# Kernel tuning notes

Hardware: AMD Instinct MI355X
Metric: run time of the kernel (lower is better)

## Reference

```python
import jax, jax.numpy as jnp
import numpy as np

B, C, G, Q, OUT = 2, 96, 32, 32, 45
M_FREQS = 12
SIGMA = 3.0


def _fourier_encode(c):
    # c: [..., 3]; log-linear frequency bank scaled by SIGMA (sigma**(j/m))
    m = M_FREQS
    freqs = SIGMA ** (jnp.arange(m, dtype=c.dtype) / m)          # [m]
    ang = 2.0 * jnp.pi * c[..., None] * freqs                    # [..., 3, m]
    enc = jnp.concatenate([jnp.sin(ang), jnp.cos(ang)], axis=-1)  # [..., 3, 2m]
    return enc.reshape(c.shape[:-1] + (3 * 2 * m,))


def setup_inputs():
    key = jax.random.key(0)
    ks = jax.random.split(key, 10)
    d = {}
    d["context_v"] = jax.random.normal(ks[0], (B, C, G, G, G), jnp.float32)
    g = jnp.arange(G, dtype=jnp.float32)
    grid = jnp.stack(jnp.meshgrid(g, g, g, indexing="ij"), axis=-1)  # [G,G,G,3]
    d["context_world_coord_grid"] = jnp.broadcast_to(grid, (B, G, G, G, 3))
    # queries strictly inside the grid so floor()+1 <= G-1
    d["query_world_coord"] = jax.random.uniform(ks[1], (B, Q, Q, Q, 3), jnp.float32, 0.0, G - 1.001)
    d["query_world_coord_mask"] = jnp.ones((B, Q, Q, Q, 1), dtype=bool)
    eye = jnp.broadcast_to(jnp.eye(4, dtype=jnp.float32), (B, 4, 4))
    d["affine_context_vox2world"] = eye
    d["affine_query_vox2world"] = eye
    d["context_vox_size_world"] = jnp.ones((B, 3), jnp.float32)
    d["query_vox_size_world"] = jnp.ones((B, 3), jnp.float32)

    n_coord = 6 + 3 * 2 * M_FREQS  # 78
    internal = C + n_coord         # 174

    def lin(k, fi, fo):
        s = 1.0 / np.sqrt(fi)
        kw, kb = jax.random.split(k)
        return (jax.random.uniform(kw, (fi, fo), jnp.float32, -s, s),
                jax.random.uniform(kb, (fo,), jnp.float32, -s, s))

    pk = jax.random.split(ks[2], 7)
    d["w00"], d["b00"] = lin(pk[0], internal, C)
    d["w01"], d["b01"] = lin(pk[1], C, C)
    d["w02"], d["b02"] = lin(pk[2], C, C)
    d["w10"], d["b10"] = lin(pk[3], internal, C)
    d["w11"], d["b11"] = lin(pk[4], C, C)
    d["w12"], d["b12"] = lin(pk[5], C, C)
    d["w_post"], d["b_post"] = lin(pk[6], C, OUT)
    return d


def reference(context_v, context_world_coord_grid, query_world_coord,
              query_world_coord_mask, affine_context_vox2world,
              affine_query_vox2world, context_vox_size_world,
              query_vox_size_world, w00, b00, w01, b01, w02, b02,
              w10, b10, w11, b11, w12, b12, w_post, b_post):
    Bq = context_v.shape[0]
    qshape = query_world_coord.shape
    qw = query_world_coord.reshape(Bq, -1, 3)          # [B,N,3]
    N = qw.shape[1]
    qm = query_world_coord_mask.reshape(Bq, -1, 1)     # [B,N,1]
    dummy = qw[:, N // 2][:, None]                      # [B,1,3]
    qw = jnp.where(qm, qw, dummy)

    inv = jnp.linalg.inv(affine_context_vox2world)
    q_vox = jnp.einsum("brc,bnc->bnr", inv[:, :3, :3], qw) + inv[:, None, :3, 3]
    bottom = jnp.floor(q_vox).astype(jnp.int32)         # [B,N,3]
    sub = q_vox - bottom.astype(q_vox.dtype)

    cvt = jnp.transpose(context_v, (0, 2, 3, 4, 1))     # [B,X,Y,Z,C]
    bidx = jnp.arange(Bq)[:, None]
    maskf = qm.astype(q_vox.dtype)
    blocks = ((w00, b00, w01, b01, w02, b02), (w10, b10, w11, b11, w12, b12))
    acc = jnp.zeros((Bq, N, w_post.shape[1]), q_vox.dtype)

    for oi in (0, 1):
        for oj in (0, 1):
            for ok in (0, 1):
                off_i = jnp.array([oi, oj, ok], dtype=bottom.dtype)
                idx = bottom + off_i                    # [B,N,3]
                feats = cvt[bidx, idx[..., 0], idx[..., 1], idx[..., 2]] * maskf  # [B,N,C]
                cw = context_world_coord_grid[bidx, idx[..., 0], idx[..., 1], idx[..., 2]]  # [B,N,3]
                off_f = off_i.astype(q_vox.dtype)
                rel = (sub - off_f + 1.0) / 2.0
                enc = _fourier_encode(rel)              # [B,N,72]
                coord = jnp.concatenate([cw, qw, enc], axis=-1) * maskf  # [B,N,78]
                y = feats
                for (wa, ba, wb, bb, wc, bc) in blocks:  # SkipMLPBlock x2
                    h = jnp.concatenate([y, coord], axis=-1)
                    h = jax.nn.silu(h @ wa + ba)
                    h = jax.nn.silu(h @ wb + bb)
                    h = jax.nn.silu(h @ wc + bc)
                    y = y + h
                pred = y @ w_post + b_post              # [B,N,OUT]
                compl = jnp.abs(1.0 - off_f)
                w_tri = jnp.prod(jnp.abs(bottom.astype(q_vox.dtype) + compl - q_vox), axis=-1, keepdims=True)
                acc = acc + w_tri * pred

    out = jnp.transpose(acc, (0, 2, 1)).reshape((Bq, w_post.shape[1]) + qshape[1:-1])
    return out
```

## Files before the change

### kernel.cpp

```cpp
#include <hip/hip_runtime.h>

#define NQv   32768
#define GSH   9216
#define NGRP  9
#define WTOT  (GSH*NGRP)
#define ASTR  104
#define CSTR  80
#define WBLK  325

typedef __attribute__((ext_vector_type(8))) short  short8;
typedef __attribute__((ext_vector_type(4))) float  float4v;

__device__ __forceinline__ float bfu2f(unsigned short u) {
  return __uint_as_float(((unsigned int)u) << 16);
}
__device__ __forceinline__ unsigned short f2bfu(float f) {
  unsigned int x = __float_as_uint(f);
  x += 0x7fffu + ((x >> 16) & 1u);
  return (unsigned short)(x >> 16);
}
__device__ __forceinline__ unsigned int rnd16(float f) {
  return __float_as_uint(f) + 0x8000u;
}
__device__ __forceinline__ unsigned int pkp(float lo, float hi) {
  return __builtin_amdgcn_perm(rnd16(hi), rnd16(lo), 0x07060302u);
}
__device__ __forceinline__ float silu_f(float x) {
  float e = __expf(-x);
  return x * __builtin_amdgcn_rcpf(1.f + e);
}
__device__ __forceinline__ int clamp31(int v) { return min(max(v, 0), 31); }

__device__ __forceinline__ void gload_lds16(const void* g, void* l) {
  typedef const __attribute__((address_space(1))) unsigned int GU;
  typedef __attribute__((address_space(3))) unsigned int LU;
  __builtin_amdgcn_global_load_lds((GU*)g, (LU*)l, 16, 0, 0);
}

__global__ __launch_bounds__(256) void prep_kernel(
    const float* __restrict__ ctxv,
    const float* __restrict__ w00, const float* __restrict__ w01,
    const float* __restrict__ w02, const float* __restrict__ w10,
    const float* __restrict__ w11, const float* __restrict__ w12,
    const float* __restrict__ wpost,
    const float* __restrict__ b00, const float* __restrict__ b10,
    unsigned short* __restrict__ ws, unsigned short* __restrict__ ctxvt)
{
  __shared__ float tile[96][65];
  const int blk0 = blockIdx.x;
  const int t = threadIdx.x;
  if (blk0 < WBLK) {
    int e = blk0 * 256 + t;
    if (e >= WTOT) {
      int e2 = e - WTOT;
      if (e2 < 192) {
        int mat = e2 / 96, ch = e2 - mat * 96;
        const float* w = mat ? w10 : w00;
        const float* bb = mat ? b10 : b00;
        float s = bb[ch];
#pragma unroll
        for (int k = 0; k < 6; ++k) s += 15.5f * w[(96 + k) * 96 + ch];
        ((float*)(ws + WTOT))[e2] = s;
      }
      return;
    }
    int g = e / GSH, r = e - g * GSH;
    int T = r >> 9, c = (r >> 3) & 63, e8 = r & 7;
    int mt = T / 3, cb = T - mt * 3;
    int ln15 = c >> 2, quad = c & 3;
    int n = mt * 16 + ln15;
    int kk = cb * 32 + quad * 8 + e8;
    const float* src; int Ksrc, Nsrc, kofs;
    switch (g) {
      case 0:  src = w00;   Ksrc = 174; Nsrc = 96; kofs = 0;  break;
      case 1:  src = w00;   Ksrc = 174; Nsrc = 96; kofs = 96; break;
      case 2:  src = w01;   Ksrc = 96;  Nsrc = 96; kofs = 0;  break;
      case 3:  src = w02;   Ksrc = 96;  Nsrc = 96; kofs = 0;  break;
      case 4:  src = w10;   Ksrc = 174; Nsrc = 96; kofs = 0;  break;
      case 5:  src = w10;   Ksrc = 174; Nsrc = 96; kofs = 96; break;
      case 6:  src = w11;   Ksrc = 96;  Nsrc = 96; kofs = 0;  break;
      case 7:  src = w12;   Ksrc = 96;  Nsrc = 96; kofs = 0;  break;
      default: src = wpost; Ksrc = 96;  Nsrc = 45; kofs = 0;  break;
    }
    int k = kofs + kk;
    float v = (k < Ksrc && n < Nsrc) ? src[k * Nsrc + n] : 0.f;
    ws[e] = f2bfu(v);
    return;
  }
  const int blk = blk0 - WBLK;
  const int b = blk >> 9, s0 = (blk & 511) << 6;
  const int cq = t >> 6, sl = t & 63;
#pragma unroll
  for (int p = 0; p < 24; ++p) {
    int c = cq + p * 4;
    tile[c][sl] = ctxv[(((size_t)(b * 96 + c)) << 15) + s0 + sl];
  }
  __syncthreads();
#pragma unroll
  for (int i = 0; i < 24; ++i) {
    int u = t + 256 * i;
    int s = u / 96, c = u - s * 96;
    ctxvt[((size_t)(b << 15) + s0 + s) * 96 + c] = f2bfu(tile[c][s]);
  }
}

template<int NM, bool INIT, bool BREG>
__device__ __forceinline__ void run_group(
    const short* __restrict__ sWp,
    const short* pA, const short8 (&Bin)[3][2],
    const float* __restrict__ bias, int biasN,
    float4v (&C)[NM][2], int lane, int rowb)
{
  const int ln15 = lane & 15, quad = lane >> 4;
  const int cidx = ((ln15 << 2) | quad) << 3;
  if (INIT) {
    if (biasN >= NM * 16) {
#pragma unroll
      for (int mt = 0; mt < NM; ++mt) {
        float4v bv = *(const float4v*)(bias + mt * 16 + quad * 4);
        C[mt][0] = bv; C[mt][1] = bv;
      }
    } else {
#pragma unroll
      for (int mt = 0; mt < NM; ++mt) {
        int c0 = mt * 16 + quad * 4;
        float4v bv;
#pragma unroll
        for (int r = 0; r < 4; ++r) bv[r] = (c0 + r < biasN) ? bias[c0 + r] : 0.f;
        C[mt][0] = bv; C[mt][1] = bv;
      }
    }
  }
  short8 Wh[3][NM];
#pragma unroll
  for (int cb = 0; cb < 3; ++cb)
#pragma unroll
    for (int mt = 0; mt < NM; ++mt)
      Wh[cb][mt] = *(const short8*)&sWp[((mt * 3 + cb) << 9) + cidx];
  short8 Bh[3][2];
  if (BREG) {
#pragma unroll
    for (int cb = 0; cb < 3; ++cb) {
      Bh[cb][0] = Bin[cb][0]; Bh[cb][1] = Bin[cb][1];
    }
  } else {
#pragma unroll
    for (int cb = 0; cb < 3; ++cb)
#pragma unroll
      for (int nt = 0; nt < 2; ++nt)
        Bh[cb][nt] = *(const short8*)&pA[(rowb + nt * 16 + ln15) * ASTR + cb * 32 + quad * 8];
  }
#pragma unroll
  for (int cb = 0; cb < 3; ++cb)
#pragma unroll
    for (int mt = 0; mt < NM; ++mt)
#pragma unroll
      for (int nt = 0; nt < 2; ++nt)
        C[mt][nt] = __builtin_amdgcn_mfma_f32_16x16x32_bf16(Wh[cb][mt], Bh[cb][nt], C[mt][nt], 0, 0, 0);
}

template<bool TRANSPOSED>
__global__ __launch_bounds__(256, 2) void decoder_kernel(
    const float* __restrict__ ctxv,
    const unsigned short* __restrict__ ctxvt,
    const float* __restrict__ qwc,
    const float* __restrict__ aff,
    const float* __restrict__ b01, const float* __restrict__ b02,
    const float* __restrict__ b11, const float* __restrict__ b12,
    const float* __restrict__ bpost,
    const unsigned short* __restrict__ ws,
    float* __restrict__ out)
{
  __shared__ __align__(16) short sY[128 * ASTR];
  __shared__ __align__(16) short sH[128 * ASTR];
  __shared__ __align__(16) short sW[GSH];
  unsigned short* sTs = (unsigned short*)sH;
  short* sC    = sH + 2304;
  int*   sqbot = (int*)(sH + 12544);
  float* sqsub = (float*)(sH + 12544 + 96);

  const int t = threadIdx.x;
  const int blk = blockIdx.x;
  const int b = blk >> 11;
  const int qbase = (blk & 2047) * 16;
  const int lane = t & 63, wid = t >> 6;
  const int ln15 = lane & 15, quad = lane >> 4;
  const int rowb = wid * 32;
  const float* badj = (const float*)(ws + WTOT);

  auto stageW = [&](int g) {
    const char* src = (const char*)ws + (size_t)g * (GSH * 2);
    char* dst = (char*)sW;
#pragma unroll
    for (int rr = 0; rr < 5; ++rr) {
      int idx = t + 256 * rr;
      if (rr < 4 || idx < 1152)
        gload_lds16(src + (size_t)idx * 16, dst + idx * 16);
    }
  };

  stageW(0);

  if (t < 16) {
    float m[4][8];
    for (int i = 0; i < 4; ++i)
      for (int j = 0; j < 4; ++j) {
        m[i][j] = aff[b * 16 + i * 4 + j];
        m[i][j + 4] = (i == j) ? 1.f : 0.f;
      }
    for (int col = 0; col < 4; ++col) {
      int piv = col; float best = fabsf(m[col][col]);
      for (int rr = col + 1; rr < 4; ++rr) {
        float v = fabsf(m[rr][col]);
        if (v > best) { best = v; piv = rr; }
      }
      if (piv != col)
        for (int j = 0; j < 8; ++j) { float tmp = m[col][j]; m[col][j] = m[piv][j]; m[piv][j] = tmp; }
      float d = 1.f / m[col][col];
      for (int j = 0; j < 8; ++j) m[col][j] *= d;
      for (int rr = 0; rr < 4; ++rr) if (rr != col) {
        float f = m[rr][col];
        for (int j = 0; j < 8; ++j) m[rr][j] -= f * m[col][j];
      }
    }
    int qi = qbase + t;
    float x = qwc[((size_t)b * NQv + qi) * 3 + 0];
    float y = qwc[((size_t)b * NQv + qi) * 3 + 1];
    float z = qwc[((size_t)b * NQv + qi) * 3 + 2];
    float v0 = m[0][4] * x + m[0][5] * y + m[0][6] * z + m[0][7];
    float v1 = m[1][4] * x + m[1][5] * y + m[1][6] * z + m[1][7];
    float v2 = m[2][4] * x + m[2][5] * y + m[2][6] * z + m[2][7];
    int i0 = (int)floorf(v0), i1 = (int)floorf(v1), i2 = (int)floorf(v2);
    sqbot[t * 3 + 0] = i0; sqbot[t * 3 + 1] = i1; sqbot[t * 3 + 2] = i2;
    sqsub[t * 3 + 0] = v0 - (float)i0; sqsub[t * 3 + 1] = v1 - (float)i1; sqsub[t * 3 + 2] = v2 - (float)i2;
  }
  __syncthreads();

#pragma unroll
  for (int i = 0; i < 3; ++i) {
    int u = lane + 64 * i;
    if (u < 144) {
      int ql = u / 36, rem = u - 36 * ql, d = rem / 12, fj = rem - 12 * d;
      int q = 4 * wid + ql;
      float sub = sqsub[q * 3 + d];
      float freq = exp2f((float)fj * 0.13208020839342968f);
#pragma unroll
      for (int off = 0; off < 2; ++off) {
        float rel = (sub - (float)off + 1.f) * 0.5f;
        float ang = 6.283185307179586f * rel * freq;
        float sn, cs; __sincosf(ang, &sn, &cs);
        int base = ((q * 3 + d) * 2 + off) * 24 + fj;
        sTs[base]      = f2bfu(sn);
        sTs[base + 12] = f2bfu(cs);
      }
    }
  }

  float wtri = 0.f;
  if (lane < 32) {
    int row = rowb + lane;
    int ql = row >> 3, cor = row & 7;
    int oi = (cor >> 2) & 1, oj = (cor >> 1) & 1, ok = cor & 1;
    float wx = oi ? sqsub[ql * 3 + 0] : 1.f - sqsub[ql * 3 + 0];
    float wy = oj ? sqsub[ql * 3 + 1] : 1.f - sqsub[ql * 3 + 1];
    float wz = ok ? sqsub[ql * 3 + 2] : 1.f - sqsub[ql * 3 + 2];
    wtri = wx * wy * wz;
  }

  {
    const int rl = lane >> 1;
    const int row = rowb + rl;
    const int ql = row >> 3, cor = row & 7;
    const int oi = (cor >> 2) & 1, oj = (cor >> 1) & 1, ok = cor & 1;
    int offv[3]; offv[0] = oi; offv[1] = oj; offv[2] = ok;
    const int cbase = (lane & 1) * 40;
    float qw3[3];
#pragma unroll
    for (int k = 0; k < 3; ++k)
      qw3[k] = qwc[((size_t)b * NQv + qbase + ql) * 3 + k];
#pragma unroll
    for (int g = 0; g < 10; ++g) {
      unsigned short hv[4];
#pragma unroll
      for (int r = 0; r < 4; ++r) {
        int ch = cbase + 4 * g + r;
        if (ch < 3) {
          float v = (float)clamp31(sqbot[ql * 3 + ch] + offv[ch]) - 15.5f;
          hv[r] = (unsigned short)(rnd16(v) >> 16);
        } else if (ch < 6) {
          float v = qw3[ch - 3] - 15.5f;
          hv[r] = (unsigned short)(rnd16(v) >> 16);
        } else if (ch < 78) {
          int i2 = ch - 6, d = i2 / 24, rr = i2 - 24 * d, sc = rr / 12, fj = rr - 12 * sc;
          hv[r] = sTs[(((ql * 3 + d) * 2 + offv[d]) * 2 + sc) * 12 + fj];
        } else hv[r] = 0;
      }
      *(uint2*)&sC[row * CSTR + cbase + 4 * g] =
          make_uint2((unsigned int)hv[0] | ((unsigned int)hv[1] << 16),
                     (unsigned int)hv[2] | ((unsigned int)hv[3] << 16));
    }
  }
  short8 Bc[3][2];
#pragma unroll
  for (int c = 0; c < 3; ++c)
#pragma unroll
    for (int nt = 0; nt < 2; ++nt)
      Bc[c][nt] = (c == 2 && quad >= 2)
                  ? (short8)0
                  : *(const short8*)&sC[(rowb + nt * 16 + ln15) * CSTR + c * 32 + quad * 8];

  {
    const int rl = lane >> 1;
    const int row = rowb + rl;
    const int ql = row >> 3, cor = row & 7;
    const int oi = (cor >> 2) & 1, oj = (cor >> 1) & 1, ok = cor & 1;
    const int jb = (lane & 1) * 48;
    const int ix = clamp31(sqbot[ql * 3 + 0] + oi);
    const int iy = clamp31(sqbot[ql * 3 + 1] + oj);
    const int iz = clamp31(sqbot[ql * 3 + 2] + ok);
    const int spat = (ix << 10) | (iy << 5) | iz;
    if (TRANSPOSED) {
      const unsigned short* src = ctxvt + ((size_t)(b << 15) + spat) * 96 + jb;
#pragma unroll
      for (int g = 0; g < 6; ++g)
        *(short8*)&sY[row * ASTR + jb + 8 * g] = *(const short8*)(src + 8 * g);
    } else {
#pragma unroll 4
      for (int g = 0; g < 12; ++g) {
        float vv[4];
#pragma unroll
        for (int r = 0; r < 4; ++r)
          vv[r] = ctxv[(((size_t)(b * 96 + jb + 4 * g + r)) << 15) + spat];
        *(uint2*)&sY[row * ASTR + jb + 4 * g] = make_uint2(pkp(vv[0], vv[1]), pkp(vv[2], vv[3]));
      }
    }
  }
  __syncthreads();

  auto epiH = [&](float4v (&C)[6][2]) {
#pragma unroll
    for (int mt = 0; mt < 6; ++mt)
#pragma unroll
      for (int nt = 0; nt < 2; ++nt) {
        int idx = (rowb + nt * 16 + ln15) * ASTR + mt * 16 + quad * 4;
        *(uint2*)&sH[idx] = make_uint2(pkp(silu_f(C[mt][nt][0]), silu_f(C[mt][nt][1])),
                                       pkp(silu_f(C[mt][nt][2]), silu_f(C[mt][nt][3])));
      }
  };
  auto epiSkip = [&](float4v (&C)[6][2]) {
#pragma unroll
    for (int mt = 0; mt < 6; ++mt)
#pragma unroll
      for (int nt = 0; nt < 2; ++nt) {
        int idx = (rowb + nt * 16 + ln15) * ASTR + mt * 16 + quad * 4;
        uint2 oh = *(uint2*)&sY[idx];
        float y0 = __uint_as_float(oh.x << 16)          + silu_f(C[mt][nt][0]);
        float y1 = __uint_as_float(oh.x & 0xffff0000u)  + silu_f(C[mt][nt][1]);
        float y2 = __uint_as_float(oh.y << 16)          + silu_f(C[mt][nt][2]);
        float y3 = __uint_as_float(oh.y & 0xffff0000u)  + silu_f(C[mt][nt][3]);
        *(uint2*)&sY[idx] = make_uint2(pkp(y0, y1), pkp(y2, y3));
      }
  };

  {
    float4v C[6][2];
    run_group<6, true , false>(sW, sY, Bc, badj,      96, C, lane, rowb);
    __syncthreads();
    stageW(1);
    __syncthreads();
    run_group<6, false, true >(sW, sY, Bc, badj,      96, C, lane, rowb);
    __syncthreads();
    stageW(2);
    epiH(C);
    __syncthreads();
    run_group<6, true , false>(sW, sH, Bc, b01,       96, C, lane, rowb);
    __syncthreads();
    stageW(3);
    epiH(C);
    __syncthreads();
    run_group<6, true , false>(sW, sH, Bc, b02,       96, C, lane, rowb);
    __syncthreads();
    stageW(4);
    epiSkip(C);
    __syncthreads();
    run_group<6, true , false>(sW, sY, Bc, badj + 96, 96, C, lane, rowb);
    __syncthreads();
    stageW(5);
    __syncthreads();
    run_group<6, false, true >(sW, sY, Bc, badj,      96, C, lane, rowb);
    __syncthreads();
    stageW(6);
    epiH(C);
    __syncthreads();
    run_group<6, true , false>(sW, sH, Bc, b11,       96, C, lane, rowb);
    __syncthreads();
    stageW(7);
    epiH(C);
    __syncthreads();
    run_group<6, true , false>(sW, sH, Bc, b12,       96, C, lane, rowb);
    __syncthreads();
    stageW(8);
    epiSkip(C);
    __syncthreads();
  }
  float* pred = (float*)sH;
  {
    float4v Cp[3][2];
    run_group<3, true, false>(sW, sY, Bc, bpost, 45, Cp, lane, rowb);
    float w0 = __shfl(wtri, ln15);
    float w1 = __shfl(wtri, 16 + ln15);
#pragma unroll
    for (int mt = 0; mt < 3; ++mt)
#pragma unroll
      for (int nt = 0; nt < 2; ++nt) {
        int row = rowb + nt * 16 + ln15, c0 = mt * 16 + quad * 4;
        float w = nt ? w1 : w0;
        float4v v = Cp[mt][nt];
        v[0] *= w; v[1] *= w; v[2] *= w; v[3] *= w;
        *(float4v*)&pred[row * 52 + c0] = v;
      }
  }
#pragma unroll
  for (int i = 0; i < 3; ++i) {
    int u = lane + 64 * i;
    if (u < 180) {
      int ql = u / 45, ch = u - ql * 45;
      float s = 0.f;
#pragma unroll
      for (int cor = 0; cor < 8; ++cor) s += pred[(rowb + ql * 8 + cor) * 52 + ch];
      out[(((size_t)(b * 45 + ch)) << 15) + qbase + wid * 4 + ql] = s;
    }
  }
}

extern "C" void kernel_launch(void* const* d_in, const int* in_sizes, int n_in,
                              void* d_out, int out_size, void* d_ws, size_t ws_size,
                              hipStream_t stream) {
  (void)in_sizes; (void)n_in; (void)out_size;
  const float* ctxv  = (const float*)d_in[0];
  const float* qwc   = (const float*)d_in[2];
  const float* aff   = (const float*)d_in[4];
  const float* w00   = (const float*)d_in[8];
  const float* b00   = (const float*)d_in[9];
  const float* w01   = (const float*)d_in[10];
  const float* b01   = (const float*)d_in[11];
  const float* w02   = (const float*)d_in[12];
  const float* b02   = (const float*)d_in[13];
  const float* w10   = (const float*)d_in[14];
  const float* b10   = (const float*)d_in[15];
  const float* w11   = (const float*)d_in[16];
  const float* b11   = (const float*)d_in[17];
  const float* w12   = (const float*)d_in[18];
  const float* b12   = (const float*)d_in[19];
  const float* wpost = (const float*)d_in[20];
  const float* bpost = (const float*)d_in[21];
  unsigned short* ws = (unsigned short*)d_ws;
  float* out = (float*)d_out;

  const size_t wbytes = (size_t)WTOT * sizeof(unsigned short) + 768;
  const size_t tbytes = (size_t)2 * 32768 * 96 * sizeof(unsigned short);
  unsigned short* ctxvt = (unsigned short*)((char*)d_ws + wbytes);
  const bool useT = ws_size >= wbytes + tbytes;

  if (useT) {
    prep_kernel<<<dim3(WBLK + 1024), dim3(256), 0, stream>>>(
        ctxv, w00, w01, w02, w10, w11, w12, wpost, b00, b10, ws, ctxvt);
    decoder_kernel<true><<<dim3(4096), dim3(256), 0, stream>>>(
        ctxv, ctxvt, qwc, aff, b01, b02, b11, b12, bpost, ws, out);
  } else {
    prep_kernel<<<dim3(WBLK), dim3(256), 0, stream>>>(
        ctxv, w00, w01, w02, w10, w11, w12, wpost, b00, b10, ws, ctxvt);
    decoder_kernel<false><<<dim3(4096), dim3(256), 0, stream>>>(
        ctxv, ctxvt, qwc, aff, b01, b02, b11, b12, bpost, ws, out);
  }
}
```

Baseline: 287.9 us.

## Share staged weight tiles across two query tiles per 512-thread block

Each block now runs 512 threads that process two independent 16-query tiles, each with its own sY/sH buffers, while sharing one staged weight buffer sW. The goal is to halve global-to-LDS weight staging per query and the number of blocks. In exchange, each __syncthreads now spans 8 waves instead of 4, and LDS per block grows. Launch bounds change from (256,2) to (512,1), which can change register allocation and occupancy.

```diff
diff --git a/kernel.cpp b/kernel.cpp
--- a/kernel.cpp
+++ b/kernel.cpp
@@ -160,7 +160,7 @@
 }
 
 template<bool TRANSPOSED>
-__global__ __launch_bounds__(256, 2) void decoder_kernel(
+__global__ __launch_bounds__(512, 1) void decoder_kernel(
     const float* __restrict__ ctxv,
     const unsigned short* __restrict__ ctxvt,
     const float* __restrict__ qwc,
@@ -171,37 +171,41 @@
     const unsigned short* __restrict__ ws,
     float* __restrict__ out)
 {
-  __shared__ __align__(16) short sY[128 * ASTR];
-  __shared__ __align__(16) short sH[128 * ASTR];
+  __shared__ __align__(16) short sY[2][128 * ASTR];
+  __shared__ __align__(16) short sH[2][128 * ASTR];
   __shared__ __align__(16) short sW[GSH];
-  unsigned short* sTs = (unsigned short*)sH;
-  short* sC    = sH + 2304;
-  int*   sqbot = (int*)(sH + 12544);
-  float* sqsub = (float*)(sH + 12544 + 96);
 
   const int t = threadIdx.x;
   const int blk = blockIdx.x;
-  const int b = blk >> 11;
-  const int qbase = (blk & 2047) * 16;
+  const int b = blk >> 10;
   const int lane = t & 63, wid = t >> 6;
+  const int tile = wid >> 2, wl = wid & 3;
+  const int qbase = (blk & 1023) * 32 + tile * 16;
   const int ln15 = lane & 15, quad = lane >> 4;
-  const int rowb = wid * 32;
+  const int rowb = wl * 32;
   const float* badj = (const float*)(ws + WTOT);
+
+  short* sYt = sY[tile];
+  short* sHt = sH[tile];
+  unsigned short* sTs = (unsigned short*)sHt;
+  short* sC    = sHt + 2304;
+  int*   sqbot = (int*)(sHt + 12544);
+  float* sqsub = (float*)(sHt + 12544 + 96);
 
   auto stageW = [&](int g) {
     const char* src = (const char*)ws + (size_t)g * (GSH * 2);
     char* dst = (char*)sW;
 #pragma unroll
-    for (int rr = 0; rr < 5; ++rr) {
-      int idx = t + 256 * rr;
-      if (rr < 4 || idx < 1152)
+    for (int rr = 0; rr < 3; ++rr) {
+      int idx = t + 512 * rr;
+      if (rr < 2 || idx < 1152)
         gload_lds16(src + (size_t)idx * 16, dst + idx * 16);
     }
   };
 
   stageW(0);
 
-  if (t < 16) {
+  if (wl == 0 && lane < 16) {
     float m[4][8];
     for (int i = 0; i < 4; ++i)
       for (int j = 0; j < 4; ++j) {
@@ -223,7 +227,7 @@
         for (int j = 0; j < 8; ++j) m[rr][j] -= f * m[col][j];
       }
     }
-    int qi = qbase + t;
+    int qi = qbase + lane;
     float x = qwc[((size_t)b * NQv + qi) * 3 + 0];
     float y = qwc[((size_t)b * NQv + qi) * 3 + 1];
     float z = qwc[((size_t)b * NQv + qi) * 3 + 2];
@@ -231,8 +235,8 @@
     float v1 = m[1][4] * x + m[1][5] * y + m[1][6] * z + m[1][7];
     float v2 = m[2][4] * x + m[2][5] * y + m[2][6] * z + m[2][7];
     int i0 = (int)floorf(v0), i1 = (int)floorf(v1), i2 = (int)floorf(v2);
-    sqbot[t * 3 + 0] = i0; sqbot[t * 3 + 1] = i1; sqbot[t * 3 + 2] = i2;
-    sqsub[t * 3 + 0] = v0 - (float)i0; sqsub[t * 3 + 1] = v1 - (float)i1; sqsub[t * 3 + 2] = v2 - (float)i2;
+    sqbot[lane * 3 + 0] = i0; sqbot[lane * 3 + 1] = i1; sqbot[lane * 3 + 2] = i2;
+    sqsub[lane * 3 + 0] = v0 - (float)i0; sqsub[lane * 3 + 1] = v1 - (float)i1; sqsub[lane * 3 + 2] = v2 - (float)i2;
   }
   __syncthreads();
 
@@ -241,7 +245,7 @@
     int u = lane + 64 * i;
     if (u < 144) {
       int ql = u / 36, rem = u - 36 * ql, d = rem / 12, fj = rem - 12 * d;
-      int q = 4 * wid + ql;
+      int q = 4 * wl + ql;
       float sub = sqsub[q * 3 + d];
       float freq = exp2f((float)fj * 0.13208020839342968f);
 #pragma unroll
@@ -323,7 +327,7 @@
       const unsigned short* src = ctxvt + ((size_t)(b << 15) + spat) * 96 + jb;
 #pragma unroll
       for (int g = 0; g < 6; ++g)
-        *(short8*)&sY[row * ASTR + jb + 8 * g] = *(const short8*)(src + 8 * g);
+        *(short8*)&sYt[row * ASTR + jb + 8 * g] = *(const short8*)(src + 8 * g);
     } else {
 #pragma unroll 4
       for (int g = 0; g < 12; ++g) {
@@ -331,7 +335,7 @@
 #pragma unroll
         for (int r = 0; r < 4; ++r)
           vv[r] = ctxv[(((size_t)(b * 96 + jb + 4 * g + r)) << 15) + spat];
-        *(uint2*)&sY[row * ASTR + jb + 4 * g] = make_uint2(pkp(vv[0], vv[1]), pkp(vv[2], vv[3]));
+        *(uint2*)&sYt[row * ASTR + jb + 4 * g] = make_uint2(pkp(vv[0], vv[1]), pkp(vv[2], vv[3]));
       }
     }
   }
@@ -343,8 +347,8 @@
 #pragma unroll
       for (int nt = 0; nt < 2; ++nt) {
         int idx = (rowb + nt * 16 + ln15) * ASTR + mt * 16 + quad * 4;
-        *(uint2*)&sH[idx] = make_uint2(pkp(silu_f(C[mt][nt][0]), silu_f(C[mt][nt][1])),
-                                       pkp(silu_f(C[mt][nt][2]), silu_f(C[mt][nt][3])));
+        *(uint2*)&sHt[idx] = make_uint2(pkp(silu_f(C[mt][nt][0]), silu_f(C[mt][nt][1])),
+                                        pkp(silu_f(C[mt][nt][2]), silu_f(C[mt][nt][3])));
       }
   };
   auto epiSkip = [&](float4v (&C)[6][2]) {
@@ -353,60 +357,60 @@
 #pragma unroll
       for (int nt = 0; nt < 2; ++nt) {
         int idx = (rowb + nt * 16 + ln15) * ASTR + mt * 16 + quad * 4;
-        uint2 oh = *(uint2*)&sY[idx];
+        uint2 oh = *(uint2*)&sYt[idx];
         float y0 = __uint_as_float(oh.x << 16)          + silu_f(C[mt][nt][0]);
         float y1 = __uint_as_float(oh.x & 0xffff0000u)  + silu_f(C[mt][nt][1]);
         float y2 = __uint_as_float(oh.y << 16)          + silu_f(C[mt][nt][2]);
         float y3 = __uint_as_float(oh.y & 0xffff0000u)  + silu_f(C[mt][nt][3]);
-        *(uint2*)&sY[idx] = make_uint2(pkp(y0, y1), pkp(y2, y3));
+        *(uint2*)&sYt[idx] = make_uint2(pkp(y0, y1), pkp(y2, y3));
       }
   };
 
   {
     float4v C[6][2];
-    run_group<6, true , false>(sW, sY, Bc, badj,      96, C, lane, rowb);
+    run_group<6, true , false>(sW, sYt, Bc, badj,      96, C, lane, rowb);
     __syncthreads();
     stageW(1);
     __syncthreads();
-    run_group<6, false, true >(sW, sY, Bc, badj,      96, C, lane, rowb);
+    run_group<6, false, true >(sW, sYt, Bc, badj,      96, C, lane, rowb);
     __syncthreads();
     stageW(2);
     epiH(C);
     __syncthreads();
-    run_group<6, true , false>(sW, sH, Bc, b01,       96, C, lane, rowb);
+    run_group<6, true , false>(sW, sHt, Bc, b01,       96, C, lane, rowb);
     __syncthreads();
     stageW(3);
     epiH(C);
     __syncthreads();
-    run_group<6, true , false>(sW, sH, Bc, b02,       96, C, lane, rowb);
+    run_group<6, true , false>(sW, sHt, Bc, b02,       96, C, lane, rowb);
     __syncthreads();
     stageW(4);
     epiSkip(C);
     __syncthreads();
-    run_group<6, true , false>(sW, sY, Bc, badj + 96, 96, C, lane, rowb);
+    run_group<6, true , false>(sW, sYt, Bc, badj + 96, 96, C, lane, rowb);
     __syncthreads();
     stageW(5);
     __syncthreads();
-    run_group<6, false, true >(sW, sY, Bc, badj,      96, C, lane, rowb);
+    run_group<6, false, true >(sW, sYt, Bc, badj,      96, C, lane, rowb);
     __syncthreads();
     stageW(6);
     epiH(C);
     __syncthreads();
-    run_group<6, true , false>(sW, sH, Bc, b11,       96, C, lane, rowb);
+    run_group<6, true , false>(sW, sHt, Bc, b11,       96, C, lane, rowb);
     __syncthreads();
     stageW(7);
     epiH(C);
     __syncthreads();
-    run_group<6, true , false>(sW, sH, Bc, b12,       96, C, lane, rowb);
+    run_group<6, true , false>(sW, sHt, Bc, b12,       96, C, lane, rowb);
     __syncthreads();
     stageW(8);
     epiSkip(C);
     __syncthreads();
   }
-  float* pred = (float*)sH;
+  float* pred = (float*)sHt;
   {
     float4v Cp[3][2];
-    run_group<3, true, false>(sW, sY, Bc, bpost, 45, Cp, lane, rowb);
+    run_group<3, true, false>(sW, sYt, Bc, bpost, 45, Cp, lane, rowb);
     float w0 = __shfl(wtri, ln15);
     float w1 = __shfl(wtri, 16 + ln15);
 #pragma unroll
@@ -428,7 +432,7 @@
       float s = 0.f;
 #pragma unroll
       for (int cor = 0; cor < 8; ++cor) s += pred[(rowb + ql * 8 + cor) * 52 + ch];
-      out[(((size_t)(b * 45 + ch)) << 15) + qbase + wid * 4 + ql] = s;
+      out[(((size_t)(b * 45 + ch)) << 15) + qbase + wl * 4 + ql] = s;
     }
   }
 }
@@ -465,12 +469,12 @@
   if (useT) {
     prep_kernel<<<dim3(WBLK + 1024), dim3(256), 0, stream>>>(
         ctxv, w00, w01, w02, w10, w11, w12, wpost, b00, b10, ws, ctxvt);
-    decoder_kernel<true><<<dim3(4096), dim3(256), 0, stream>>>(
+    decoder_kernel<true><<<dim3(2048), dim3(512), 0, stream>>>(
         ctxv, ctxvt, qwc, aff, b01, b02, b11, b12, bpost, ws, out);
   } else {
     prep_kernel<<<dim3(WBLK), dim3(256), 0, stream>>>(
         ctxv, w00, w01, w02, w10, w11, w12, wpost, b00, b10, ws, ctxvt);
-    decoder_kernel<false><<<dim3(4096), dim3(256), 0, stream>>>(
+    decoder_kernel<false><<<dim3(2048), dim3(512), 0, stream>>>(
         ctxv, ctxvt, qwc, aff, b01, b02, b11, b12, bpost, ws, out);
   }
 }
```

New measurement: 313.8 us. 1.09x slower.
